# Kernel tuning notes

Hardware: AMD Instinct MI355X
Metric: run time of the kernel (lower is better)

The kernel has to match this reference:

```python
import jax, jax.numpy as jnp
import numpy as np

INPUT_SIZE = 256
HIDDEN_SIZE = 256


def setup_inputs() -> dict:
    key = jax.random.key(0)
    k_x, k_wxh, k_whh = jax.random.split(key, 3)
    x = jax.random.normal(k_x, (64, 2048, INPUT_SIZE), dtype=jnp.float32)
    # torch nn.Linear weights: [out_features, in_features]
    W_xh = jax.random.normal(k_wxh, (HIDDEN_SIZE, INPUT_SIZE), dtype=jnp.float32) / np.sqrt(INPUT_SIZE)
    W_hh = jax.random.normal(k_whh, (HIDDEN_SIZE, HIDDEN_SIZE), dtype=jnp.float32) / np.sqrt(HIDDEN_SIZE)
    b_h = jnp.zeros((HIDDEN_SIZE,), dtype=jnp.float32)
    return {"x": x, "W_xh": W_xh, "W_hh": W_hh, "b_h": b_h}


def reference(x, W_xh, W_hh, b_h):
    # x: [B, T, D]; h_t = relu(x_t @ W_xh^T + h_{t-1} @ W_hh^T + b_h)
    B, T, _ = x.shape
    # Precompute input projection for all timesteps in one GEMM (same math).
    xproj = jnp.einsum('btd,hd->bth', x, W_xh) + b_h  # [B, T, H]

    def step(h, xp_t):
        h_new = jax.nn.relu(xp_t + h @ W_hh.T)
        return h_new, h_new

    h0 = jnp.zeros((B, HIDDEN_SIZE), dtype=x.dtype)
    # scan over time axis: move T to leading dim
    _, hs = jax.lax.scan(step, h0, jnp.swapaxes(xproj, 0, 1))  # hs: [T, B, H]
    return jnp.swapaxes(hs, 0, 1)  # [B, T, H]
```

## Files before the change

kernel.cpp:

```cpp
#include <hip/hip_runtime.h>

#define BATCH 64
#define SEQT  2048
#define DIM   256
#define HID   256

typedef _Float16 half_t;
typedef _Float16 half2_t __attribute__((ext_vector_type(2)));
typedef _Float16 half4_t __attribute__((ext_vector_type(4)));
typedef _Float16 half8_t __attribute__((ext_vector_type(8)));
typedef float    float4_t __attribute__((ext_vector_type(4)));

__device__ __forceinline__ half8_t cvt8(float4_t a, float4_t b) {
  half8_t r;
  r[0] = (half_t)a[0]; r[1] = (half_t)a[1]; r[2] = (half_t)a[2]; r[3] = (half_t)a[3];
  r[4] = (half_t)b[0]; r[5] = (half_t)b[1]; r[6] = (half_t)b[2]; r[7] = (half_t)b[3];
  return r;
}
#define H2X(v, c) __builtin_shufflevector((v), (v), 2*(c), 2*(c)+1)

template<int CTRL>
__device__ __forceinline__ float dpp_mov(float a) {
  int t = __builtin_amdgcn_mov_dpp(__builtin_bit_cast(int, a), CTRL, 0xF, 0xF, true);
  return __builtin_bit_cast(float, t);
}

__global__ __launch_bounds__(256) void cvt_w_kernel(
    const float* __restrict__ W, half_t* __restrict__ Wh)
{
  const int i = (blockIdx.x * 256 + threadIdx.x) * 4;
  float4_t v = *(const float4_t*)(W + i);
  half4_t o; o[0]=(half_t)v[0]; o[1]=(half_t)v[1]; o[2]=(half_t)v[2]; o[3]=(half_t)v[3];
  *(half4_t*)(Wh + i) = o;
}

__global__ __launch_bounds__(256) void xproj_f16_kernel(
    const float* __restrict__ x, const half_t* __restrict__ Wh,
    const float* __restrict__ bh, float* __restrict__ out)
{
  const int lane = threadIdx.x & 63;
  const int wave = threadIdx.x >> 6;
  const int r16  = lane & 15;
  const int kg   = lane >> 4;
  const long m0  = (long)blockIdx.x * 64 + wave * 16;

  half8_t a[8];
  const float* xr = x + (m0 + r16) * (long)DIM + kg * 8;
  #pragma unroll
  for (int kf = 0; kf < 8; ++kf) {
    float4_t x0 = *(const float4_t*)(xr + kf * 32);
    float4_t x1 = *(const float4_t*)(xr + kf * 32 + 4);
    a[kf] = cvt8(x0, x1);
  }

  #pragma unroll 2
  for (int nt = 0; nt < 16; ++nt) {
    const half_t* wr = Wh + (nt * 16 + r16) * (long)DIM + kg * 8;
    float bb = bh[nt * 16 + r16];
    float4_t acc = {bb, bb, bb, bb};
    #pragma unroll
    for (int kf = 0; kf < 8; ++kf) {
      half8_t bfrag = *(const half8_t*)(wr + kf * 32);
      acc = __builtin_amdgcn_mfma_f32_16x16x32_f16(a[kf], bfrag, acc, 0, 0, 0);
    }
    float* op = out + (m0 + kg * 4) * (long)HID + nt * 16 + r16;
    #pragma unroll
    for (int r = 0; r < 4; ++r) op[(long)r * HID] = acc[r];
  }
}

__global__ __launch_bounds__(256) void xproj_kernel(
    const float* __restrict__ x, const float* __restrict__ Wxh,
    const float* __restrict__ bh, float* __restrict__ out)
{
  const int lane = threadIdx.x & 63;
  const int wave = threadIdx.x >> 6;
  const int r16  = lane & 15;
  const int kg   = lane >> 4;
  const long m0  = (long)blockIdx.x * 64 + wave * 16;

  half8_t a[8];
  const float* xr = x + (m0 + r16) * (long)DIM + kg * 8;
  #pragma unroll
  for (int kf = 0; kf < 8; ++kf) {
    float4_t x0 = *(const float4_t*)(xr + kf * 32);
    float4_t x1 = *(const float4_t*)(xr + kf * 32 + 4);
    a[kf] = cvt8(x0, x1);
  }
  for (int nt = 0; nt < 16; ++nt) {
    const float* wr = Wxh + (nt * 16 + r16) * (long)DIM + kg * 8;
    float bb = bh[nt * 16 + r16];
    float4_t acc = {bb, bb, bb, bb};
    #pragma unroll
    for (int kf = 0; kf < 8; ++kf) {
      float4_t w0 = *(const float4_t*)(wr + kf * 32);
      float4_t w1 = *(const float4_t*)(wr + kf * 32 + 4);
      acc = __builtin_amdgcn_mfma_f32_16x16x32_f16(a[kf], cvt8(w0, w1), acc, 0, 0, 0);
    }
    float* op = out + (m0 + kg * 4) * (long)HID + nt * 16 + r16;
    #pragma unroll
    for (int r = 0; r < 4; ++r) op[(long)r * HID] = acc[r];
  }
}

#define RNN_BAR() asm volatile("s_waitcnt lgkmcnt(0)\n\ts_barrier" ::: "memory")

#define RNN_STEP(U, XQ)                                                        \
  {                                                                            \
    const int t = t4 + (U);                                                    \
         \
    const int tp = (t + 4 < T) ? (t + 4) : (T - 1);                            \
    float xnew = outp[(long)tp * HID];                                         \
    half8_t hv[4];                                                             \
    _Pragma("unroll")                                                          \
    for (int s = 0; s < 4; ++s)                                                \
      hv[s] = *(const half8_t*)(hraw[(U) & 1] + rb + 16 * s);                  \
    float a[8] = {0.f, 0.f, 0.f, 0.f, 0.f, 0.f, 0.f, 0.f};                     \
    _Pragma("unroll")                                                          \
    for (int s = 0; s < 4; ++s) {                                              \
      _Pragma("unroll")                                                        \
      for (int i = 0; i < 8; ++i) {                                            \
        a[i] = __builtin_amdgcn_fdot2(H2X(w8[i][s], 0), H2X(hv[s], 0), a[i], false); \
        a[i] = __builtin_amdgcn_fdot2(H2X(w8[i][s], 1), H2X(hv[s], 1), a[i], false); \
        a[i] = __builtin_amdgcn_fdot2(H2X(w8[i][s], 2), H2X(hv[s], 2), a[i], false); \
        a[i] = __builtin_amdgcn_fdot2(H2X(w8[i][s], 3), H2X(hv[s], 3), a[i], false); \
      }                                                                        \
    }                                                                          \
          \
    float b0, b1, b2, b3, c0, c1, fin;                                         \
    {               \
      float r0 = s4 ? a[0] : a[4];                                             \
      float r1 = s4 ? a[1] : a[5];                                             \
      float r2 = s4 ? a[2] : a[6];                                             \
      float r3 = s4 ? a[3] : a[7];                                             \
      b0 = (s4 ? a[4] : a[0]) + dpp_mov<0x141>(r0);                            \
      b1 = (s4 ? a[5] : a[1]) + dpp_mov<0x141>(r1);                            \
      b2 = (s4 ? a[6] : a[2]) + dpp_mov<0x141>(r2);                            \
      b3 = (s4 ? a[7] : a[3]) + dpp_mov<0x141>(r3);                            \
    }                                                                          \
    {                            \
      float r0 = s1 ? b0 : b1;                                                 \
      float r1 = s1 ? b2 : b3;                                                 \
      c0 = (s1 ? b1 : b0) + dpp_mov<0xB1>(r0);                                 \
      c1 = (s1 ? b3 : b2) + dpp_mov<0xB1>(r1);                                 \
    }                                                                          \
    {                            \
      float r = s2 ? c0 : c1;                                                  \
      fin = (s2 ? c1 : c0) + dpp_mov<0x4E>(r);                                 \
    }                                                                          \
    float y = fmaxf(fin + (XQ), 0.f);                                          \
    outp[(long)t * HID] = y;                                                   \
    *(half_t*)(hraw[((U) & 1) ^ 1] + hwb) = (half_t)y;                         \
    XQ = xnew;                                                                 \
    RNN_BAR();                                                                 \
  }

__global__ __launch_bounds__(256, 1) void rnn_kernel(
    const float* __restrict__ Whh, float* __restrict__ out, int T)
{
  __shared__ alignas(128) unsigned char hraw[2][8 * 80];

  const int tid = threadIdx.x;
  const int l   = tid & 63;
  const int w   = tid >> 6;
  const int g   = l & 7;
  const int jo  = w * 8 + (l >> 3);
  const int j0  = jo * 8;
  const int rb  = g * 80;
  const int jown = w * 64 + l;
  const int hwb = ((jown >> 5) * 80 + (jown & 31) * 2);
  const bool s4 = (l & 4) != 0;
  const bool s1 = (l & 1) != 0;
  const bool s2 = (l & 2) != 0;
  float* outp = out + (long)blockIdx.x * SEQT * HID + jown;

  half8_t w8[8][4];
  #pragma unroll
  for (int i = 0; i < 8; ++i) {
    const float* wr = Whh + (long)(j0 + i) * HID + g * 32;
    #pragma unroll
    for (int s = 0; s < 4; ++s) {
      float4_t v0 = *(const float4_t*)(wr + s * 8);
      float4_t v1 = *(const float4_t*)(wr + s * 8 + 4);
      w8[i][s] = cvt8(v0, v1);
    }
  }

  if (tid < 160) ((float*)hraw[0])[tid] = 0.f;

  float xq0 = outp[0L * HID];
  float xq1 = outp[1L * HID];
  float xq2 = outp[2L * HID];
  float xq3 = outp[3L * HID];
  RNN_BAR();

  #pragma unroll 1
  for (int t4 = 0; t4 < T; t4 += 4) {
    RNN_STEP(0, xq0)
    RNN_STEP(1, xq1)
    RNN_STEP(2, xq2)
    RNN_STEP(3, xq3)
  }
}

extern "C" void kernel_launch(void* const* d_in, const int* in_sizes, int n_in,
                              void* d_out, int out_size, void* d_ws, size_t ws_size,
                              hipStream_t stream) {
  const float* x   = (const float*)d_in[0];
  const float* Wxh = (const float*)d_in[1];
  const float* Whh = (const float*)d_in[2];
  const float* bh  = (const float*)d_in[3];
  float* out = (float*)d_out;

  if (ws_size >= (size_t)(DIM * HID * sizeof(half_t))) {
    half_t* Wh = (half_t*)d_ws;
    cvt_w_kernel<<<dim3((DIM * HID) / 1024), dim3(256), 0, stream>>>(Wxh, Wh);
    xproj_f16_kernel<<<dim3((BATCH * SEQT) / 64), dim3(256), 0, stream>>>(x, Wh, bh, out);
  } else {
    xproj_kernel<<<dim3((BATCH * SEQT) / 64), dim3(256), 0, stream>>>(x, Wxh, bh, out);
  }
  rnn_kernel<<<dim3(BATCH), dim3(256), 0, stream>>>(Whh, out, SEQT);
}
```

Baseline: 1.018 ms.

## Split recurrent matvec across 512 threads with four rows per thread

The recurrent kernel now launches 512 threads per batch element instead of 256. Each thread holds 4 rows of W_hh (32 k-elements each) instead of 8, which halves the serial fdot2 chain on the per-timestep critical path. The cross-lane reduction is rebuilt as a shorter DPP tree where lane pairs end up redundantly holding the same output. The cost is twice as many waves meeting at every per-step barrier, plus duplicated global loads and stores of identical values by paired lanes.

```diff
diff --git a/kernel.cpp b/kernel.cpp
--- a/kernel.cpp
+++ b/kernel.cpp
@@ -115,39 +115,34 @@
     _Pragma("unroll")                                                          \
     for (int s = 0; s < 4; ++s)                                                \
       hv[s] = *(const half8_t*)(hraw[(U) & 1] + rb + 16 * s);                  \
-    float a[8] = {0.f, 0.f, 0.f, 0.f, 0.f, 0.f, 0.f, 0.f};                     \
+    float a0 = 0.f, a1 = 0.f, a2 = 0.f, a3 = 0.f;                              \
     _Pragma("unroll")                                                          \
     for (int s = 0; s < 4; ++s) {                                              \
-      _Pragma("unroll")                                                        \
-      for (int i = 0; i < 8; ++i) {                                            \
-        a[i] = __builtin_amdgcn_fdot2(H2X(w8[i][s], 0), H2X(hv[s], 0), a[i], false); \
-        a[i] = __builtin_amdgcn_fdot2(H2X(w8[i][s], 1), H2X(hv[s], 1), a[i], false); \
-        a[i] = __builtin_amdgcn_fdot2(H2X(w8[i][s], 2), H2X(hv[s], 2), a[i], false); \
-        a[i] = __builtin_amdgcn_fdot2(H2X(w8[i][s], 3), H2X(hv[s], 3), a[i], false); \
-      }                                                                        \
+      a0 = __builtin_amdgcn_fdot2(H2X(w8[0][s], 0), H2X(hv[s], 0), a0, false); \
+      a0 = __builtin_amdgcn_fdot2(H2X(w8[0][s], 1), H2X(hv[s], 1), a0, false); \
+      a0 = __builtin_amdgcn_fdot2(H2X(w8[0][s], 2), H2X(hv[s], 2), a0, false); \
+      a0 = __builtin_amdgcn_fdot2(H2X(w8[0][s], 3), H2X(hv[s], 3), a0, false); \
+      a1 = __builtin_amdgcn_fdot2(H2X(w8[1][s], 0), H2X(hv[s], 0), a1, false); \
+      a1 = __builtin_amdgcn_fdot2(H2X(w8[1][s], 1), H2X(hv[s], 1), a1, false); \
+      a1 = __builtin_amdgcn_fdot2(H2X(w8[1][s], 2), H2X(hv[s], 2), a1, false); \
+      a1 = __builtin_amdgcn_fdot2(H2X(w8[1][s], 3), H2X(hv[s], 3), a1, false); \
+      a2 = __builtin_amdgcn_fdot2(H2X(w8[2][s], 0), H2X(hv[s], 0), a2, false); \
+      a2 = __builtin_amdgcn_fdot2(H2X(w8[2][s], 1), H2X(hv[s], 1), a2, false); \
+      a2 = __builtin_amdgcn_fdot2(H2X(w8[2][s], 2), H2X(hv[s], 2), a2, false); \
+      a2 = __builtin_amdgcn_fdot2(H2X(w8[2][s], 3), H2X(hv[s], 3), a2, false); \
+      a3 = __builtin_amdgcn_fdot2(H2X(w8[3][s], 0), H2X(hv[s], 0), a3, false); \
+      a3 = __builtin_amdgcn_fdot2(H2X(w8[3][s], 1), H2X(hv[s], 1), a3, false); \
+      a3 = __builtin_amdgcn_fdot2(H2X(w8[3][s], 2), H2X(hv[s], 2), a3, false); \
+      a3 = __builtin_amdgcn_fdot2(H2X(w8[3][s], 3), H2X(hv[s], 3), a3, false); \
     }                                                                          \
-          \
-    float b0, b1, b2, b3, c0, c1, fin;                                         \
-    {               \
-      float r0 = s4 ? a[0] : a[4];                                             \
-      float r1 = s4 ? a[1] : a[5];                                             \
-      float r2 = s4 ? a[2] : a[6];                                             \
-      float r3 = s4 ? a[3] : a[7];                                             \
-      b0 = (s4 ? a[4] : a[0]) + dpp_mov<0x141>(r0);                            \
-      b1 = (s4 ? a[5] : a[1]) + dpp_mov<0x141>(r1);                            \
-      b2 = (s4 ? a[6] : a[2]) + dpp_mov<0x141>(r2);                            \
-      b3 = (s4 ? a[7] : a[3]) + dpp_mov<0x141>(r3);                            \
-    }                                                                          \
-    {                            \
-      float r0 = s1 ? b0 : b1;                                                 \
-      float r1 = s1 ? b2 : b3;                                                 \
-      c0 = (s1 ? b1 : b0) + dpp_mov<0xB1>(r0);                                 \
-      c1 = (s1 ? b3 : b2) + dpp_mov<0xB1>(r1);                                 \
-    }                                                                          \
-    {                            \
-      float r = s2 ? c0 : c1;                                                  \
-      fin = (s2 ? c1 : c0) + dpp_mov<0x4E>(r);                                 \
-    }                                                                          \
+        \
+    float r0 = kA ? a0 : a2;                 \
+    float r1 = kA ? a1 : a3;                                                   \
+    float b0 = (kA ? a2 : a0) + dpp_mov<0x141>(r0);                            \
+    float b1 = (kA ? a3 : a1) + dpp_mov<0x141>(r1);                            \
+    float rB = kB ? b0 : b1;                 \
+    float c  = (kB ? b1 : b0) + dpp_mov<0x4E>(rB);                             \
+    float fin = c + dpp_mov<0xB1>(c);            \
     float y = fmaxf(fin + (XQ), 0.f);                                          \
     outp[(long)t * HID] = y;                                                   \
     *(half_t*)(hraw[((U) & 1) ^ 1] + hwb) = (half_t)y;                         \
@@ -155,7 +150,7 @@
     RNN_BAR();                                                                 \
   }
 
-__global__ __launch_bounds__(256, 1) void rnn_kernel(
+__global__ __launch_bounds__(512, 1) void rnn_kernel(
     const float* __restrict__ Whh, float* __restrict__ out, int T)
 {
   __shared__ alignas(128) unsigned char hraw[2][8 * 80];
@@ -164,19 +159,17 @@
   const int l   = tid & 63;
   const int w   = tid >> 6;
   const int g   = l & 7;
-  const int jo  = w * 8 + (l >> 3);
-  const int j0  = jo * 8;
+  const int j0  = w * 32 + (l >> 3) * 4;
   const int rb  = g * 80;
-  const int jown = w * 64 + l;
+  const int jown = j0 + ((l >> 1) & 3);
   const int hwb = ((jown >> 5) * 80 + (jown & 31) * 2);
-  const bool s4 = (l & 4) != 0;
-  const bool s1 = (l & 1) != 0;
-  const bool s2 = (l & 2) != 0;
+  const bool kA = (l & 4) != 0;
+  const bool kB = (l & 2) != 0;
   float* outp = out + (long)blockIdx.x * SEQT * HID + jown;
 
-  half8_t w8[8][4];
+  half8_t w8[4][4];
   #pragma unroll
-  for (int i = 0; i < 8; ++i) {
+  for (int i = 0; i < 4; ++i) {
     const float* wr = Whh + (long)(j0 + i) * HID + g * 32;
     #pragma unroll
     for (int s = 0; s < 4; ++s) {
@@ -219,5 +212,5 @@
   } else {
     xproj_kernel<<<dim3((BATCH * SEQT) / 64), dim3(256), 0, stream>>>(x, Wxh, bh, out);
   }
-  rnn_kernel<<<dim3(BATCH), dim3(256), 0, stream>>>(Whh, out, SEQT);
-}
+  rnn_kernel<<<dim3(BATCH), dim3(512), 0, stream>>>(Whh, out, SEQT);
+}
```

Result: faster. 989.7 us (-2.8%).
